# Optimization experiments

Hardware: AMD Instinct MI355X
Metric: run time of the kernel (lower is better)

The kernel has to match this reference:

```python
import jax, jax.numpy as jnp
import numpy as np

N_NODES = 65536
DEGREE = 16
N_EDGES = N_NODES * DEGREE
IN_CH = 128
HEADS = 4
OUT_CH = 16
NEG_SLOPE = 0.2


def setup_inputs() -> dict:
    key = jax.random.key(0)
    k1, k2, k3, k4, k5, k6 = jax.random.split(key, 6)
    csr_row_ptr = jnp.arange(N_NODES + 1, dtype=jnp.int64) * DEGREE
    csr_col_ind = jax.random.randint(k1, (N_EDGES,), 0, N_NODES, dtype=jnp.int64)
    sample_count = jnp.ones((N_NODES,), dtype=jnp.int64)
    x_neighboor = jax.random.normal(k2, (N_NODES, IN_CH), dtype=jnp.float32)
    x_target = jax.random.normal(k3, (N_NODES, IN_CH), dtype=jnp.float32)
    # xavier-ish init scales
    W = jax.random.normal(k4, (IN_CH, HEADS * OUT_CH), dtype=jnp.float32) * (2.0 / (IN_CH + HEADS * OUT_CH)) ** 0.5
    attn_l = jax.random.normal(k5, (HEADS, OUT_CH), dtype=jnp.float32) * 0.1
    attn_r = jax.random.normal(k6, (HEADS, OUT_CH), dtype=jnp.float32) * 0.1
    bias = jnp.zeros((HEADS * OUT_CH,), dtype=jnp.float32)
    return {"csr_row_ptr": csr_row_ptr, "csr_col_ind": csr_col_ind,
            "sample_count": sample_count, "x_neighboor": x_neighboor,
            "x_target": x_target, "W": W, "attn_l": attn_l,
            "attn_r": attn_r, "bias": bias}


def reference(csr_row_ptr, csr_col_ind, sample_count, x_neighboor, x_target, W, attn_l, attn_r, bias):
    N = csr_row_ptr.shape[0] - 1
    E = csr_col_ind.shape[0]
    H, C = attn_l.shape
    # linear projection: [Nn, in] @ [in, H*C] -> [Nn, H, C]
    feat = (x_neighboor @ W).reshape(-1, H, C)
    feat_target = feat[:N]
    el = jnp.sum(feat_target * attn_l[None], axis=-1)  # [N, H]
    er = jnp.sum(feat * attn_r[None], axis=-1)         # [Nn, H]
    # row id of each edge from CSR row pointers
    row_id = jnp.searchsorted(csr_row_ptr, jnp.arange(E), side='right') - 1  # [E]
    # spadd_gat: per-edge score = el[row] + er[col], then leaky relu
    w = el[row_id] + er[csr_col_ind]                   # [E, H]
    w = jnp.where(w >= 0, w, NEG_SLOPE * w)
    # segment (per-row) softmax over edges, numerically stable
    wmax = jax.lax.stop_gradient(jax.ops.segment_max(w, row_id, num_segments=N))
    ew = jnp.exp(w - wmax[row_id])
    denom = jax.ops.segment_sum(ew, row_id, num_segments=N)
    alpha = ew / denom[row_id]                         # [E, H]
    # weighted sparse aggregation (gspmm): y[r] = sum_e alpha[e] * feat[col[e]]
    y = jax.ops.segment_sum(alpha[:, :, None] * feat[csr_col_ind], row_id, num_segments=N)  # [N, H, C]
    y = y + bias.reshape(1, H, C)
    return y.reshape(N, H * C)
```

## Files before the change

kernel.cpp:

```cpp
#include <hip/hip_runtime.h>
#include <hip/hip_bf16.h>

#define IN_CH 128
#define HC 64
#define NEG_SLOPE 0.2f

typedef __attribute__((ext_vector_type(8))) short short8;
typedef __attribute__((ext_vector_type(4))) float floatx4;

__device__ __forceinline__ unsigned short f2bf_rne(float f) {
    unsigned int u = __float_as_uint(f);
    u += 0x7fffu + ((u >> 16) & 1u);
    return (unsigned short)(u >> 16);
}
__device__ __forceinline__ float bf2f(unsigned short u) {
    union { unsigned int i; float f; } v; v.i = ((unsigned int)u) << 16; return v.f;
}

__global__ __launch_bounds__(256, 4) void feat_gemm_kernel(
    const float* __restrict__ xf,
    const float* __restrict__ Wf,
    const float* __restrict__ attn_l,
    const float* __restrict__ attn_r,
    unsigned short* __restrict__ feat,
    float* __restrict__ elr,
    int N)
{
    __shared__ unsigned short lw[10240];
    const int tid = threadIdx.x;
    const int row0 = blockIdx.x * 64;
    const int w    = tid >> 6;
    const int lane = tid & 63;
    const int m    = lane & 15;
    const int q    = lane >> 4;

    const float* xrow = xf + (size_t)(row0 + w * 16 + m) * IN_CH + q * 8;
    float4 xa[4][2];
    #pragma unroll
    for (int c = 0; c < 4; ++c) {
        xa[c][0] = *(const float4*)(xrow + c * 32);
        xa[c][1] = *(const float4*)(xrow + c * 32 + 4);
    }

    #pragma unroll
    for (int i = 0; i < 8; ++i) {
        int fi = i * 256 + tid;
        float4 v = ((const float4*)Wf)[fi];
        int k  = fi >> 4;
        int n0 = (fi & 15) * 4;
        int c = k >> 5, qq = (k & 31) >> 3, j = k & 7;
        int ct = n0 >> 4, np0 = n0 & 15;
        float e[4] = {v.x, v.y, v.z, v.w};
        #pragma unroll
        for (int t2 = 0; t2 < 4; ++t2) {
            int ln = qq * 16 + np0 + t2;
            lw[((ct * 4 + c) * 64 + ln) * 8 + j] = f2bf_rne(e[t2]);
        }
    }

    if (tid < 128) {
        int k = tid;
        int c = k >> 5, qq = (k & 31) >> 3, j = k & 7;
        float wa[8];
        #pragma unroll
        for (int h = 0; h < 4; ++h) {
            float sl = 0.f, sr = 0.f;
            #pragma unroll
            for (int cc = 0; cc < 16; ++cc) {
                float wkc = Wf[k * HC + h * 16 + cc];
                sl += wkc * attn_l[h * 16 + cc];
                sr += wkc * attn_r[h * 16 + cc];
            }
            wa[h] = sl; wa[4 + h] = sr;
        }
        #pragma unroll
        for (int n = 0; n < 16; ++n) {
            int ln = qq * 16 + n;
            lw[8192 + (c * 64 + ln) * 8 + j] = (n < 8) ? f2bf_rne(wa[n]) : (unsigned short)0;
        }
    }

    short8 afrag[4];
    #pragma unroll
    for (int c = 0; c < 4; ++c) {
        union { unsigned int u[4]; short8 s; } pk;
        pk.u[0] = (unsigned int)f2bf_rne(xa[c][0].x) | ((unsigned int)f2bf_rne(xa[c][0].y) << 16);
        pk.u[1] = (unsigned int)f2bf_rne(xa[c][0].z) | ((unsigned int)f2bf_rne(xa[c][0].w) << 16);
        pk.u[2] = (unsigned int)f2bf_rne(xa[c][1].x) | ((unsigned int)f2bf_rne(xa[c][1].y) << 16);
        pk.u[3] = (unsigned int)f2bf_rne(xa[c][1].z) | ((unsigned int)f2bf_rne(xa[c][1].w) << 16);
        afrag[c] = pk.s;
    }

    __syncthreads();

    floatx4 acc[4], accA;
    #pragma unroll
    for (int ct = 0; ct < 4; ++ct) acc[ct] = (floatx4){0.f, 0.f, 0.f, 0.f};
    accA = (floatx4){0.f, 0.f, 0.f, 0.f};

    #pragma unroll
    for (int c = 0; c < 4; ++c) {
        short8 wafrag = *(const short8*)&lw[8192 + (c * 64 + lane) * 8];
        accA = __builtin_amdgcn_mfma_f32_16x16x32_bf16(afrag[c], wafrag, accA, 0, 0, 0);
        #pragma unroll
        for (int ct = 0; ct < 4; ++ct) {
            short8 bfrag = *(const short8*)&lw[((ct * 4 + c) * 64 + lane) * 8];
            acc[ct] = __builtin_amdgcn_mfma_f32_16x16x32_bf16(afrag[c], bfrag, acc[ct], 0, 0, 0);
        }
    }

    #pragma unroll
    for (int ct = 0; ct < 4; ++ct) {
        #pragma unroll
        for (int r = 0; r < 4; ++r) {
            int row = row0 + w * 16 + q * 4 + r;
            feat[(size_t)row * HC + ct * 16 + m] = f2bf_rne(acc[ct][r]);
        }
    }
    if (m < 8) {
        #pragma unroll
        for (int r = 0; r < 4; ++r) {
            int row = row0 + w * 16 + q * 4 + r;
            elr[(size_t)row * 8 + m] = accA[r];
        }
    }
}

__global__ __launch_bounds__(256) void gat_aggregate_kernel(
    const int* __restrict__ row_ptr32,
    const int* __restrict__ col_ind32,
    const unsigned short* __restrict__ feat,
    const float* __restrict__ elr,
    const float* __restrict__ bias,
    float* __restrict__ out,
    int N)
{
    const int lane = threadIdx.x & 63;
    const int node = blockIdx.x * 4 + (threadIdx.x >> 6);
    if (node >= N) return;

    const bool idx64 = (row_ptr32[1] != 16);
    int start, deg;
    if (idx64) {
        start = row_ptr32[2 * node];
        deg   = row_ptr32[2 * node + 2] - start;
    } else {
        start = row_ptr32[node];
        deg   = row_ptr32[node + 1] - start;
    }

    const int e = lane & 15;
    const int h = lane >> 4;
    int colv = 0;
    if (lane < 16 && lane < deg) {
        int ei = start + lane;
        colv = idx64 ? col_ind32[2 * ei] : col_ind32[ei];
    }

    const int r0  = __builtin_amdgcn_readlane(colv, 0);
    const int r1  = __builtin_amdgcn_readlane(colv, 1);
    const int r2  = __builtin_amdgcn_readlane(colv, 2);
    const int r3  = __builtin_amdgcn_readlane(colv, 3);
    const int r4  = __builtin_amdgcn_readlane(colv, 4);
    const int r5  = __builtin_amdgcn_readlane(colv, 5);
    const int r6  = __builtin_amdgcn_readlane(colv, 6);
    const int r7  = __builtin_amdgcn_readlane(colv, 7);
    const int r8  = __builtin_amdgcn_readlane(colv, 8);
    const int r9  = __builtin_amdgcn_readlane(colv, 9);
    const int r10 = __builtin_amdgcn_readlane(colv, 10);
    const int r11 = __builtin_amdgcn_readlane(colv, 11);
    const int r12 = __builtin_amdgcn_readlane(colv, 12);
    const int r13 = __builtin_amdgcn_readlane(colv, 13);
    const int r14 = __builtin_amdgcn_readlane(colv, 14);
    const int r15 = __builtin_amdgcn_readlane(colv, 15);

    unsigned short fv0, fv1, fv2, fv3, fv4, fv5, fv6, fv7;
    unsigned short fv8, fv9, fv10, fv11, fv12, fv13, fv14, fv15;
#define GATHER(dst, r) dst = feat[(size_t)(r) * HC + lane];
    GATHER(fv0,  r0)  GATHER(fv1,  r1)  GATHER(fv2,  r2)  GATHER(fv3,  r3)
    GATHER(fv4,  r4)  GATHER(fv5,  r5)  GATHER(fv6,  r6)  GATHER(fv7,  r7)
    GATHER(fv8,  r8)  GATHER(fv9,  r9)  GATHER(fv10, r10) GATHER(fv11, r11)
    GATHER(fv12, r12) GATHER(fv13, r13) GATHER(fv14, r14) GATHER(fv15, r15)
#undef GATHER

    int cole = __shfl(colv, e, 64);
    float w;
    if (e < deg) {
        float ww = elr[(size_t)node * 8 + h] + elr[(size_t)cole * 8 + 4 + h];
        w = (ww >= 0.f) ? ww : NEG_SLOPE * ww;
    } else {
        w = -INFINITY;
    }
    float m = w;
    #pragma unroll
    for (int o = 8; o >= 1; o >>= 1) m = fmaxf(m, __shfl_xor(m, o, 16));
    float ew = (e < deg) ? __expf(w - m) : 0.f;
    float s = ew;
    #pragma unroll
    for (int o = 8; o >= 1; o >>= 1) s += __shfl_xor(s, o, 16);
    float alpha = (s > 0.f) ? (ew / s) : 0.f;

    const int abase = lane & 48;
    float acc = 0.f;
#define ACCUM(g, fv) \
    { float a = __shfl(alpha, abase + (g), 64); acc += a * bf2f(fv); }
    ACCUM(0,  fv0)  ACCUM(1,  fv1)  ACCUM(2,  fv2)  ACCUM(3,  fv3)
    ACCUM(4,  fv4)  ACCUM(5,  fv5)  ACCUM(6,  fv6)  ACCUM(7,  fv7)
    ACCUM(8,  fv8)  ACCUM(9,  fv9)  ACCUM(10, fv10) ACCUM(11, fv11)
    ACCUM(12, fv12) ACCUM(13, fv13) ACCUM(14, fv14) ACCUM(15, fv15)
#undef ACCUM
    acc += bias[lane];
    out[(size_t)node * HC + lane] = acc;
}

extern "C" void kernel_launch(void* const* d_in, const int* in_sizes, int n_in,
                              void* d_out, int out_size, void* d_ws, size_t ws_size,
                              hipStream_t stream) {
    const int* row_ptr      = (const int*)d_in[0];
    const int* col_ind      = (const int*)d_in[1];
    const float* x          = (const float*)d_in[3];
    const float* W          = (const float*)d_in[5];
    const float* attn_l     = (const float*)d_in[6];
    const float* attn_r     = (const float*)d_in[7];
    const float* bias       = (const float*)d_in[8];

    const int N = out_size / HC;

    unsigned short* feat = (unsigned short*)d_ws;
    float* elr = (float*)((char*)d_ws + (size_t)N * HC * sizeof(unsigned short));

    feat_gemm_kernel<<<N / 64, 256, 0, stream>>>(x, W, attn_l, attn_r, feat, elr, N);
    gat_aggregate_kernel<<<(N + 3) / 4, 256, 0, stream>>>(row_ptr, col_ind, feat, elr, bias,
                                                          (float*)d_out, N);
}
```

Measured before the change: 146.9 us.

## Process four nodes per wavefront in GAT aggregation with degree-16 fast path

Result: no change. 145.9 us (-0.6%).

```diff
diff --git a/kernel.cpp b/kernel.cpp
--- a/kernel.cpp
+++ b/kernel.cpp
@@ -126,28 +126,14 @@
     }
 }
 
-__global__ __launch_bounds__(256) void gat_aggregate_kernel(
-    const int* __restrict__ row_ptr32,
-    const int* __restrict__ col_ind32,
-    const unsigned short* __restrict__ feat,
-    const float* __restrict__ elr,
-    const float* __restrict__ bias,
-    float* __restrict__ out,
-    int N)
+__device__ void gat_one(
+    const int* __restrict__ row_ptr32, const int* __restrict__ col_ind32,
+    const unsigned short* __restrict__ feat, const float* __restrict__ elr,
+    float bv, float* __restrict__ out, int node, int lane, bool idx64)
 {
-    const int lane = threadIdx.x & 63;
-    const int node = blockIdx.x * 4 + (threadIdx.x >> 6);
-    if (node >= N) return;
-
-    const bool idx64 = (row_ptr32[1] != 16);
     int start, deg;
-    if (idx64) {
-        start = row_ptr32[2 * node];
-        deg   = row_ptr32[2 * node + 2] - start;
-    } else {
-        start = row_ptr32[node];
-        deg   = row_ptr32[node + 1] - start;
-    }
+    if (idx64) { start = row_ptr32[2 * node]; deg = row_ptr32[2 * node + 2] - start; }
+    else       { start = row_ptr32[node];     deg = row_ptr32[node + 1] - start; }
 
     const int e = lane & 15;
     const int h = lane >> 4;
@@ -156,7 +142,6 @@
         int ei = start + lane;
         colv = idx64 ? col_ind32[2 * ei] : col_ind32[ei];
     }
-
     const int r0  = __builtin_amdgcn_readlane(colv, 0);
     const int r1  = __builtin_amdgcn_readlane(colv, 1);
     const int r2  = __builtin_amdgcn_readlane(colv, 2);
@@ -202,15 +187,122 @@
 
     const int abase = lane & 48;
     float acc = 0.f;
-#define ACCUM(g, fv) \
-    { float a = __shfl(alpha, abase + (g), 64); acc += a * bf2f(fv); }
+#define ACCUM(g, fv) { float a = __shfl(alpha, abase + (g), 64); acc += a * bf2f(fv); }
     ACCUM(0,  fv0)  ACCUM(1,  fv1)  ACCUM(2,  fv2)  ACCUM(3,  fv3)
     ACCUM(4,  fv4)  ACCUM(5,  fv5)  ACCUM(6,  fv6)  ACCUM(7,  fv7)
     ACCUM(8,  fv8)  ACCUM(9,  fv9)  ACCUM(10, fv10) ACCUM(11, fv11)
     ACCUM(12, fv12) ACCUM(13, fv13) ACCUM(14, fv14) ACCUM(15, fv15)
 #undef ACCUM
-    acc += bias[lane];
-    out[(size_t)node * HC + lane] = acc;
+    out[(size_t)node * HC + lane] = acc + bv;
+}
+
+__global__ __launch_bounds__(256) void gat_aggregate_kernel(
+    const int* __restrict__ row_ptr32,
+    const int* __restrict__ col_ind32,
+    const unsigned short* __restrict__ feat,
+    const float* __restrict__ elr,
+    const float* __restrict__ bias,
+    float* __restrict__ out,
+    int N)
+{
+    const int lane = threadIdx.x & 63;
+    const int n0   = (blockIdx.x * 4 + (threadIdx.x >> 6)) * 4;
+    if (n0 >= N) return;
+
+    const bool idx64 = (row_ptr32[1] != 16);
+    const float bv = bias[lane];
+
+    int rpv = 0;
+    if (lane < 5) rpv = idx64 ? row_ptr32[2 * (n0 + lane)] : row_ptr32[n0 + lane];
+    const int s0 = __builtin_amdgcn_readlane(rpv, 0);
+    const int s1 = __builtin_amdgcn_readlane(rpv, 1);
+    const int s2 = __builtin_amdgcn_readlane(rpv, 2);
+    const int s3 = __builtin_amdgcn_readlane(rpv, 3);
+    const int s4 = __builtin_amdgcn_readlane(rpv, 4);
+    const bool fast = (n0 + 3 < N) &&
+                      (s1 - s0 == 16) && (s2 - s1 == 16) &&
+                      (s3 - s2 == 16) && (s4 - s3 == 16);
+
+    if (!fast) {
+        #pragma unroll 1
+        for (int k = 0; k < 4; ++k)
+            if (n0 + k < N)
+                gat_one(row_ptr32, col_ind32, feat, elr, bv, out, n0 + k, lane, idx64);
+        return;
+    }
+
+    int colv = idx64 ? col_ind32[2 * (s0 + lane)] : col_ind32[s0 + lane];
+
+    float elv = 0.f;
+    if (lane < 32) elv = elr[((size_t)n0 + (lane >> 3)) * 8 + (lane & 7)];
+
+#define RL4(a,b,c,d) \
+    const int r##a = __builtin_amdgcn_readlane(colv, a); \
+    const int r##b = __builtin_amdgcn_readlane(colv, b); \
+    const int r##c = __builtin_amdgcn_readlane(colv, c); \
+    const int r##d = __builtin_amdgcn_readlane(colv, d);
+    RL4(0,1,2,3)     RL4(4,5,6,7)     RL4(8,9,10,11)   RL4(12,13,14,15)
+    RL4(16,17,18,19) RL4(20,21,22,23) RL4(24,25,26,27) RL4(28,29,30,31)
+    RL4(32,33,34,35) RL4(36,37,38,39) RL4(40,41,42,43) RL4(44,45,46,47)
+    RL4(48,49,50,51) RL4(52,53,54,55) RL4(56,57,58,59) RL4(60,61,62,63)
+#undef RL4
+
+#define G4(a,b,c,d) \
+    unsigned short f##a = feat[(size_t)r##a * HC + lane]; \
+    unsigned short f##b = feat[(size_t)r##b * HC + lane]; \
+    unsigned short f##c = feat[(size_t)r##c * HC + lane]; \
+    unsigned short f##d = feat[(size_t)r##d * HC + lane];
+    G4(0,1,2,3)     G4(4,5,6,7)     G4(8,9,10,11)   G4(12,13,14,15)
+    G4(16,17,18,19) G4(20,21,22,23) G4(24,25,26,27) G4(28,29,30,31)
+    G4(32,33,34,35) G4(36,37,38,39) G4(40,41,42,43) G4(44,45,46,47)
+    G4(48,49,50,51) G4(52,53,54,55) G4(56,57,58,59) G4(60,61,62,63)
+#undef G4
+
+    const int e = lane & 15;
+    const int h = lane >> 4;
+    const int abase = lane & 48;
+
+#define DO_NODE(K, F0,F1,F2,F3,F4,F5,F6,F7,F8,F9,F10,F11,F12,F13,F14,F15) { \
+    int cole = __shfl(colv, (K) * 16 + e, 64); \
+    float el = __shfl(elv, (K) * 8 + h, 64); \
+    float ww = el + elr[(size_t)cole * 8 + 4 + h]; \
+    float wv = (ww >= 0.f) ? ww : NEG_SLOPE * ww; \
+    float mm = wv; \
+    mm = fmaxf(mm, __shfl_xor(mm, 8, 16)); \
+    mm = fmaxf(mm, __shfl_xor(mm, 4, 16)); \
+    mm = fmaxf(mm, __shfl_xor(mm, 2, 16)); \
+    mm = fmaxf(mm, __shfl_xor(mm, 1, 16)); \
+    float ew = __expf(wv - mm); \
+    float ss = ew; \
+    ss += __shfl_xor(ss, 8, 16); \
+    ss += __shfl_xor(ss, 4, 16); \
+    ss += __shfl_xor(ss, 2, 16); \
+    ss += __shfl_xor(ss, 1, 16); \
+    float alpha = ew / ss; \
+    float acc = 0.f; float aa; \
+    aa = __shfl(alpha, abase + 0,  64); acc += aa * bf2f(F0); \
+    aa = __shfl(alpha, abase + 1,  64); acc += aa * bf2f(F1); \
+    aa = __shfl(alpha, abase + 2,  64); acc += aa * bf2f(F2); \
+    aa = __shfl(alpha, abase + 3,  64); acc += aa * bf2f(F3); \
+    aa = __shfl(alpha, abase + 4,  64); acc += aa * bf2f(F4); \
+    aa = __shfl(alpha, abase + 5,  64); acc += aa * bf2f(F5); \
+    aa = __shfl(alpha, abase + 6,  64); acc += aa * bf2f(F6); \
+    aa = __shfl(alpha, abase + 7,  64); acc += aa * bf2f(F7); \
+    aa = __shfl(alpha, abase + 8,  64); acc += aa * bf2f(F8); \
+    aa = __shfl(alpha, abase + 9,  64); acc += aa * bf2f(F9); \
+    aa = __shfl(alpha, abase + 10, 64); acc += aa * bf2f(F10); \
+    aa = __shfl(alpha, abase + 11, 64); acc += aa * bf2f(F11); \
+    aa = __shfl(alpha, abase + 12, 64); acc += aa * bf2f(F12); \
+    aa = __shfl(alpha, abase + 13, 64); acc += aa * bf2f(F13); \
+    aa = __shfl(alpha, abase + 14, 64); acc += aa * bf2f(F14); \
+    aa = __shfl(alpha, abase + 15, 64); acc += aa * bf2f(F15); \
+    out[(size_t)(n0 + (K)) * HC + lane] = acc + bv; \
+}
+    DO_NODE(0, f0,f1,f2,f3,f4,f5,f6,f7,f8,f9,f10,f11,f12,f13,f14,f15)
+    DO_NODE(1, f16,f17,f18,f19,f20,f21,f22,f23,f24,f25,f26,f27,f28,f29,f30,f31)
+    DO_NODE(2, f32,f33,f34,f35,f36,f37,f38,f39,f40,f41,f42,f43,f44,f45,f46,f47)
+    DO_NODE(3, f48,f49,f50,f51,f52,f53,f54,f55,f56,f57,f58,f59,f60,f61,f62,f63)
+#undef DO_NODE
 }
 
 extern "C" void kernel_launch(void* const* d_in, const int* in_sizes, int n_in,
@@ -230,6 +322,6 @@
     float* elr = (float*)((char*)d_ws + (size_t)N * HC * sizeof(unsigned short));
 
     feat_gemm_kernel<<<N / 64, 256, 0, stream>>>(x, W, attn_l, attn_r, feat, elr, N);
-    gat_aggregate_kernel<<<(N + 3) / 4, 256, 0, stream>>>(row_ptr, col_ind, feat, elr, bias,
-                                                          (float*)d_out, N);
-}
+    gat_aggregate_kernel<<<(N + 15) / 16, 256, 0, stream>>>(row_ptr, col_ind, feat, elr, bias,
+                                                            (float*)d_out, N);
+}
```
